# Kernel tuning notes

Hardware: AMD Instinct MI355X
Metric: run time of the kernel (lower is better)

## Reference

```python
import jax, jax.numpy as jnp
import numpy as np

K = 1024  # number of superpixel ids (matches fill_max of superpixel)

@jax.custom_vjp
def smooth_square(x):
    return x * x

def _ss_fwd(x):
    return x * x, x

def _ss_bwd(x, g):
    # gradient of square with input clipped to [-1, 1]
    return (g * 2.0 * jnp.clip(x, -1.0, 1.0),)

smooth_square.defvjp(_ss_fwd, _ss_bwd)

def setup_inputs() -> dict:
    key = jax.random.key(0)
    k1, k2 = jax.random.split(key)
    D, H, W = 64, 1024, 1024
    embedding = jax.random.normal(k1, (D, H, W), dtype=jnp.float32)
    superpixel = jax.random.randint(k2, (H, W), 0, K, dtype=jnp.int64)
    return {"embedding": embedding, "superpixel": superpixel}

def reference(embedding, superpixel):
    # embedding: D x H x W float, superpixel: H x W int
    D = embedding.shape[0]
    sp = superpixel.reshape(-1)                      # N = H*W
    x = embedding.reshape(D, -1)                     # D x N
    ones = jnp.ones(sp.shape, dtype=x.dtype)
    counts = jax.ops.segment_sum(ones, sp, num_segments=K)        # K
    sums = jax.ops.segment_sum(x.T, sp, num_segments=K)           # K x D
    mean = sums / jnp.maximum(counts, 1.0)[:, None]                # K x D
    dev = x - mean[sp].T                              # D x N, scores - per-segment mean
    # sum over all segments of D*variance*count == sum of squared deviations
    return smooth_square(dev).sum()
```

## Files before the change

### kernel.cpp

```cpp
#include <hip/hip_runtime.h>
#include <stdint.h>

#define K_SEG 1024
#define D_CH 64
#define DG 2
#define CHUNK 32768


__global__ void zero_ws_kernel(uint32_t* counts, float* sums, double* totals) {
    int i = blockIdx.x * blockDim.x + threadIdx.x;
    if (i == 0) { totals[0] = 0.0; totals[1] = 0.0; }
    if (i < K_SEG) counts[i] = 0u;
    int stride = gridDim.x * blockDim.x;
    for (int j = i; j < K_SEG * D_CH; j += stride) sums[j] = 0.0f;
}

__global__ void detect_layout_kernel(const int* __restrict__ sp_words, int* flag) {
    int t = threadIdx.x;
    int odd = sp_words[2 * t + 1];
    unsigned long long b = __ballot(odd == 0);
    if (t == 0) *flag = (b == ~0ULL) ? 1 : 0;
}

__global__ void prep_sp_kernel(const int* __restrict__ sp_words,
                               const int* __restrict__ flag,
                               uint16_t* __restrict__ sp16,
                               uint32_t* __restrict__ counts, int N) {
    __shared__ uint32_t lcnt[K_SEG];
    for (int i = threadIdx.x; i < K_SEG; i += blockDim.x) lcnt[i] = 0u;
    __syncthreads();
    const bool wide = (*flag != 0);
    int stride = gridDim.x * blockDim.x;
    for (int n = blockIdx.x * blockDim.x + threadIdx.x; n < N; n += stride) {
        int v = wide ? sp_words[2 * n] : sp_words[n];
        v &= (K_SEG - 1);
        sp16[n] = (uint16_t)v;
        atomicAdd(&lcnt[v], 1u);
    }
    __syncthreads();
    for (int i = threadIdx.x; i < K_SEG; i += blockDim.x) {
        uint32_t c = lcnt[i];
        if (c) atomicAdd(&counts[i], c);
    }
}

__global__ void __launch_bounds__(256)
accum_kernel(const float* __restrict__ emb, const uint16_t* __restrict__ sp16,
             float* __restrict__ sums, double* __restrict__ totals, int N) {
    __shared__ float lsum[4][DG * K_SEG];
    const int t = threadIdx.x;
    float* tile = lsum[t >> 6];
    {
        float* lflat = &lsum[0][0];
        for (int i = t; i < 4 * DG * K_SEG; i += 256) lflat[i] = 0.0f;
    }
    __syncthreads();

    const int base = blockIdx.x * CHUNK;
    const int d0 = blockIdx.y * DG;
    const float* e0 = emb + (size_t)d0 * N;
    const float* e1 = emb + (size_t)(d0 + 1) * N;
    float acc = 0.0f;

    #pragma unroll 2
    for (int it = 0; it < CHUNK / 1024; ++it) {
        const int p = base + it * 1024 + t * 4;
        if (p + 4 <= N) {
            const ushort4 k4 = *reinterpret_cast<const ushort4*>(sp16 + p);
            const float4 v0 = *reinterpret_cast<const float4*>(e0 + p);
            const float4 v1 = *reinterpret_cast<const float4*>(e1 + p);
            acc += v0.x * v0.x + v0.y * v0.y + v0.z * v0.z + v0.w * v0.w;
            acc += v1.x * v1.x + v1.y * v1.y + v1.z * v1.z + v1.w * v1.w;
            tile[k4.x] += v0.x;
            tile[k4.y] += v0.y;
            tile[k4.z] += v0.z;
            tile[k4.w] += v0.w;
            tile[K_SEG + k4.x] += v1.x;
            tile[K_SEG + k4.y] += v1.y;
            tile[K_SEG + k4.z] += v1.z;
            tile[K_SEG + k4.w] += v1.w;
        }
    }
    __syncthreads();

    for (int i = t; i < DG * K_SEG; i += 256) {
        float s = lsum[0][i] + lsum[1][i] + lsum[2][i] + lsum[3][i];
        if (s != 0.0f) atomicAdd(&sums[(size_t)d0 * K_SEG + i], s);
    }

    #pragma unroll
    for (int off = 32; off; off >>= 1) acc += __shfl_down(acc, off, 64);
    __shared__ float wsum[4];
    if ((t & 63) == 0) wsum[t >> 6] = acc;
    __syncthreads();
    if (t == 0) {
        double b = (double)wsum[0] + (double)wsum[1] + (double)wsum[2] + (double)wsum[3];
        atomicAdd(totals, b);
    }
}

__global__ void finalize_partial_kernel(const float* __restrict__ sums,
                                        const uint32_t* __restrict__ counts,
                                        double* __restrict__ totals) {
    const int t = threadIdx.x;
    int i0 = blockIdx.x * blockDim.x + t;
    int stride = gridDim.x * blockDim.x;
    double acc = 0.0;
    for (int i = i0; i < D_CH * K_SEG; i += stride) {
        float c = (float)counts[i & (K_SEG - 1)];
        float s = sums[i];
        float inv = 1.0f / fmaxf(c, 1.0f);
        acc += (double)(s * s) * (double)inv;
    }
    __shared__ double sacc[256];
    sacc[t] = acc;
    __syncthreads();
    for (int off = 128; off; off >>= 1) {
        if (t < off) sacc[t] += sacc[t + off];
        __syncthreads();
    }
    if (t == 0) atomicAdd(&totals[1], sacc[0]);
}

__global__ void final_write_kernel(const double* __restrict__ totals,
                                   float* __restrict__ out) {
    out[0] = (float)(totals[0] - totals[1]);
}

extern "C" void kernel_launch(void* const* d_in, const int* in_sizes, int n_in,
                              void* d_out, int out_size, void* d_ws, size_t ws_size,
                              hipStream_t stream) {
    const float* emb = (const float*)d_in[0];
    const int* spw = (const int*)d_in[1];
    const int N = in_sizes[1];

    char* ws = (char*)d_ws;
    double* totals = (double*)(ws + 0);
    int* flag = (int*)(ws + 64);
    uint32_t* counts = (uint32_t*)(ws + 256);
    float* sums = (float*)(ws + 4352);
    uint16_t* sp16 = (uint16_t*)(ws + 266496);

    zero_ws_kernel<<<64, 256, 0, stream>>>(counts, sums, totals);
    detect_layout_kernel<<<1, 64, 0, stream>>>(spw, flag);
    prep_sp_kernel<<<512, 256, 0, stream>>>(spw, flag, sp16, counts, N);

    dim3 grid((N + CHUNK - 1) / CHUNK, D_CH / DG);
    accum_kernel<<<grid, 256, 0, stream>>>(emb, sp16, sums, totals, N);

    finalize_partial_kernel<<<64, 256, 0, stream>>>(sums, counts, totals);
    final_write_kernel<<<1, 1, 0, stream>>>(totals, (float*)d_out);
}
```

Before: 84.23 us.

## Fold layout detection and final write into neighbours, pack LDS bins as float2

Layout detection moves into the prep kernel, and the final write moves into the finalize kernel through a last-block ticket, removing two tiny launches. The accumulation kernel now keeps its two channel sums per segment in a single float2 shared bin, so each element needs one read-modify-write instead of two. The grid is transposed so adjacent blocks share a spatial chunk of superpixel ids, and the unroll factor is raised. Each block now repeats the detection loads, the ticket relies on fences for correctness, and float2 LDS scatter may see different bank conflicts.

After: 83.08 us. About the same (-1.4%).

```diff
diff --git a/kernel.cpp b/kernel.cpp
--- a/kernel.cpp
+++ b/kernel.cpp
@@ -7,29 +7,28 @@
 #define CHUNK 32768
 
 
-__global__ void zero_ws_kernel(uint32_t* counts, float* sums, double* totals) {
+__global__ void zero_ws_kernel(uint32_t* counts, float* sums, double* totals,
+                               uint32_t* ticket) {
     int i = blockIdx.x * blockDim.x + threadIdx.x;
-    if (i == 0) { totals[0] = 0.0; totals[1] = 0.0; }
+    if (i == 0) { totals[0] = 0.0; totals[1] = 0.0; *ticket = 0u; }
     if (i < K_SEG) counts[i] = 0u;
     int stride = gridDim.x * blockDim.x;
     for (int j = i; j < K_SEG * D_CH; j += stride) sums[j] = 0.0f;
 }
 
-__global__ void detect_layout_kernel(const int* __restrict__ sp_words, int* flag) {
-    int t = threadIdx.x;
-    int odd = sp_words[2 * t + 1];
-    unsigned long long b = __ballot(odd == 0);
-    if (t == 0) *flag = (b == ~0ULL) ? 1 : 0;
-}
-
 __global__ void prep_sp_kernel(const int* __restrict__ sp_words,
-                               const int* __restrict__ flag,
                                uint16_t* __restrict__ sp16,
                                uint32_t* __restrict__ counts, int N) {
     __shared__ uint32_t lcnt[K_SEG];
+    __shared__ int wideflag;
     for (int i = threadIdx.x; i < K_SEG; i += blockDim.x) lcnt[i] = 0u;
+    if (threadIdx.x < 64) {
+        int odd = sp_words[2 * threadIdx.x + 1];
+        unsigned long long b = __ballot(odd == 0);
+        if (threadIdx.x == 0) wideflag = (b == ~0ULL) ? 1 : 0;
+    }
     __syncthreads();
-    const bool wide = (*flag != 0);
+    const bool wide = (wideflag != 0);
     int stride = gridDim.x * blockDim.x;
     for (int n = blockIdx.x * blockDim.x + threadIdx.x; n < N; n += stride) {
         int v = wide ? sp_words[2 * n] : sp_words[n];
@@ -47,22 +46,22 @@
 __global__ void __launch_bounds__(256)
 accum_kernel(const float* __restrict__ emb, const uint16_t* __restrict__ sp16,
              float* __restrict__ sums, double* __restrict__ totals, int N) {
-    __shared__ float lsum[4][DG * K_SEG];
+    __shared__ float2 lsum[4][K_SEG];
     const int t = threadIdx.x;
-    float* tile = lsum[t >> 6];
+    float2* tile = lsum[t >> 6];
     {
-        float* lflat = &lsum[0][0];
-        for (int i = t; i < 4 * DG * K_SEG; i += 256) lflat[i] = 0.0f;
+        float2* lflat = &lsum[0][0];
+        for (int i = t; i < 4 * K_SEG; i += 256) lflat[i] = make_float2(0.0f, 0.0f);
     }
     __syncthreads();
 
-    const int base = blockIdx.x * CHUNK;
-    const int d0 = blockIdx.y * DG;
+    const int d0 = blockIdx.x * DG;
+    const int base = blockIdx.y * CHUNK;
     const float* e0 = emb + (size_t)d0 * N;
     const float* e1 = emb + (size_t)(d0 + 1) * N;
     float acc = 0.0f;
 
-    #pragma unroll 2
+    #pragma unroll 4
     for (int it = 0; it < CHUNK / 1024; ++it) {
         const int p = base + it * 1024 + t * 4;
         if (p + 4 <= N) {
@@ -71,21 +70,21 @@
             const float4 v1 = *reinterpret_cast<const float4*>(e1 + p);
             acc += v0.x * v0.x + v0.y * v0.y + v0.z * v0.z + v0.w * v0.w;
             acc += v1.x * v1.x + v1.y * v1.y + v1.z * v1.z + v1.w * v1.w;
-            tile[k4.x] += v0.x;
-            tile[k4.y] += v0.y;
-            tile[k4.z] += v0.z;
-            tile[k4.w] += v0.w;
-            tile[K_SEG + k4.x] += v1.x;
-            tile[K_SEG + k4.y] += v1.y;
-            tile[K_SEG + k4.z] += v1.z;
-            tile[K_SEG + k4.w] += v1.w;
+            float2 o;
+            o = tile[k4.x]; o.x += v0.x; o.y += v1.x; tile[k4.x] = o;
+            o = tile[k4.y]; o.x += v0.y; o.y += v1.y; tile[k4.y] = o;
+            o = tile[k4.z]; o.x += v0.z; o.y += v1.z; tile[k4.z] = o;
+            o = tile[k4.w]; o.x += v0.w; o.y += v1.w; tile[k4.w] = o;
         }
     }
     __syncthreads();
 
-    for (int i = t; i < DG * K_SEG; i += 256) {
-        float s = lsum[0][i] + lsum[1][i] + lsum[2][i] + lsum[3][i];
-        if (s != 0.0f) atomicAdd(&sums[(size_t)d0 * K_SEG + i], s);
+    for (int k = t; k < K_SEG; k += 256) {
+        float2 s0 = lsum[0][k], s1 = lsum[1][k], s2 = lsum[2][k], s3 = lsum[3][k];
+        float sx = s0.x + s1.x + s2.x + s3.x;
+        float sy = s0.y + s1.y + s2.y + s3.y;
+        atomicAdd(&sums[(size_t)d0 * K_SEG + k], sx);
+        atomicAdd(&sums[(size_t)(d0 + 1) * K_SEG + k], sy);
     }
 
     #pragma unroll
@@ -99,9 +98,11 @@
     }
 }
 
-__global__ void finalize_partial_kernel(const float* __restrict__ sums,
-                                        const uint32_t* __restrict__ counts,
-                                        double* __restrict__ totals) {
+__global__ void finalize_kernel(const float* __restrict__ sums,
+                                const uint32_t* __restrict__ counts,
+                                double* __restrict__ totals,
+                                uint32_t* __restrict__ ticket,
+                                float* __restrict__ out) {
     const int t = threadIdx.x;
     int i0 = blockIdx.x * blockDim.x + t;
     int stride = gridDim.x * blockDim.x;
@@ -109,8 +110,7 @@
     for (int i = i0; i < D_CH * K_SEG; i += stride) {
         float c = (float)counts[i & (K_SEG - 1)];
         float s = sums[i];
-        float inv = 1.0f / fmaxf(c, 1.0f);
-        acc += (double)(s * s) * (double)inv;
+        acc += (double)(s * s) / (double)fmaxf(c, 1.0f);
     }
     __shared__ double sacc[256];
     sacc[t] = acc;
@@ -119,12 +119,20 @@
         if (t < off) sacc[t] += sacc[t + off];
         __syncthreads();
     }
-    if (t == 0) atomicAdd(&totals[1], sacc[0]);
-}
-
-__global__ void final_write_kernel(const double* __restrict__ totals,
-                                   float* __restrict__ out) {
-    out[0] = (float)(totals[0] - totals[1]);
+    __shared__ int last;
+    if (t == 0) {
+        atomicAdd(&totals[1], sacc[0]);
+        __threadfence();
+        uint32_t r = atomicAdd(ticket, 1u);
+        last = (r == gridDim.x - 1) ? 1 : 0;
+    }
+    __syncthreads();
+    if (last && t == 0) {
+        __threadfence();
+        double t0 = atomicAdd(&totals[0], 0.0);
+        double t1 = atomicAdd(&totals[1], 0.0);
+        out[0] = (float)(t0 - t1);
+    }
 }
 
 extern "C" void kernel_launch(void* const* d_in, const int* in_sizes, int n_in,
@@ -136,18 +144,17 @@
 
     char* ws = (char*)d_ws;
     double* totals = (double*)(ws + 0);
-    int* flag = (int*)(ws + 64);
+    uint32_t* ticket = (uint32_t*)(ws + 64);
     uint32_t* counts = (uint32_t*)(ws + 256);
     float* sums = (float*)(ws + 4352);
     uint16_t* sp16 = (uint16_t*)(ws + 266496);
 
-    zero_ws_kernel<<<64, 256, 0, stream>>>(counts, sums, totals);
-    detect_layout_kernel<<<1, 64, 0, stream>>>(spw, flag);
-    prep_sp_kernel<<<512, 256, 0, stream>>>(spw, flag, sp16, counts, N);
+    zero_ws_kernel<<<64, 256, 0, stream>>>(counts, sums, totals, ticket);
+    prep_sp_kernel<<<512, 256, 0, stream>>>(spw, sp16, counts, N);
 
-    dim3 grid((N + CHUNK - 1) / CHUNK, D_CH / DG);
+    dim3 grid(D_CH / DG, (N + CHUNK - 1) / CHUNK);
     accum_kernel<<<grid, 256, 0, stream>>>(emb, sp16, sums, totals, N);
 
-    finalize_partial_kernel<<<64, 256, 0, stream>>>(sums, counts, totals);
-    final_write_kernel<<<1, 1, 0, stream>>>(totals, (float*)d_out);
+    finalize_kernel<<<64, 256, 0, stream>>>(sums, counts, totals, ticket,
+                                            (float*)d_out);
 }
```
